# Performance work log

Hardware: AMD Instinct MI355X
Metric: run time of the kernel (lower is better)

The kernel has to match this reference:

```python
import jax, jax.numpy as jnp
import numpy as np

DEPTH = 18                     # levels 0..17 of a complete binary tree
N = 2 ** DEPTH - 1             # 262143 nodes, node n's children are 2n+1, 2n+2


def setup_inputs() -> dict:
    key = jax.random.key(0)
    ks = jax.random.split(key, 9)
    V, X, H, C = 32000, 128, 128, 5
    s = 0.05  # weight scale to keep activations in a sane range
    return {
        "x_ids": jax.random.randint(ks[0], (N,), 0, V),
        "mask": jax.random.randint(ks[1], (N,), 0, 2),
        "emb_table": jax.random.normal(ks[2], (V, X), jnp.float32),
        "W_iou": jax.random.normal(ks[3], (X, 3 * H), jnp.float32) * s,
        "U_iou": jax.random.normal(ks[4], (H, 3 * H), jnp.float32) * s,
        "b_iou": jnp.zeros((3 * H,), jnp.float32),
        "W_f": jax.random.normal(ks[5], (X, H), jnp.float32) * s,
        "U_f": jax.random.normal(ks[6], (H, H), jnp.float32) * s,
        "b_f": jnp.zeros((H,), jnp.float32),
        "W_out": jax.random.normal(ks[7], (H, C), jnp.float32) * s,
        "b_out": jnp.zeros((C,), jnp.float32),
    }


def reference(x_ids, mask, emb_table, W_iou, U_iou, b_iou, W_f, U_f, b_f, W_out, b_out):
    H = U_f.shape[0]
    # input_module: embeds = Embedding(x * mask)
    embeds = emb_table[x_ids * mask]                    # [N, X]
    # cell_module.precompute_input_values: per-node input projections
    x_iou = embeds @ W_iou + b_iou                      # [N, 3H]
    x_f = embeds @ W_f + b_f                            # [N, H]

    levels_h = [None] * DEPTH
    levels_c = [None] * DEPTH
    # dgl.prop_nodes_topo: leaves -> root, one synchronized level at a time
    for d in range(DEPTH - 1, -1, -1):
        s0, n = 2 ** d - 1, 2 ** d                      # level-d node range [s0, s0+n)
        iou = x_iou[s0:s0 + n]
        if d < DEPTH - 1:
            # children of level-d node s0+i are contiguous at level d+1: 2i, 2i+1
            h_ch = levels_h[d + 1].reshape(n, 2, H)
            c_ch = levels_c[d + 1].reshape(n, 2, H)
            iou = iou + h_ch.sum(axis=1) @ U_iou        # child-sum of h
            f = jax.nn.sigmoid(x_f[s0:s0 + n][:, None, :] + h_ch @ U_f)  # [n,2,H]
            fc = (f * c_ch).sum(axis=1)
        else:
            fc = jnp.zeros((n, H), iou.dtype)
        i, o, u = jnp.split(iou, 3, axis=-1)
        c = jax.nn.sigmoid(i) * jnp.tanh(u) + fc
        h = jax.nn.sigmoid(o) * jnp.tanh(c)
        levels_h[d] = h
        levels_c[d] = c

    h_all = jnp.concatenate(levels_h, axis=0)           # [N, H], node-index order
    # output_module: per-node linear readout
    return h_all @ W_out + b_out                        # [N, C]
```

## Files before the change

kernel.cpp:

```cpp
#include <hip/hip_runtime.h>

#define DEPTH 18
#define NN ((1 << DEPTH) - 1)

typedef __attribute__((ext_vector_type(8))) short short8;
typedef __attribute__((ext_vector_type(4))) float f32x4;

__device__ __forceinline__ float sigm_(float x) { return 1.f / (1.f + __expf(-x)); }
__device__ __forceinline__ float tanh_(float x) { float e = __expf(2.f * x); return 1.f - 2.f / (e + 1.f); }
__device__ __forceinline__ unsigned short f2bf(float f) {
    union { float f; unsigned int u; } v; v.f = f;
    unsigned int r = (v.u + 0x7fffu + ((v.u >> 16) & 1u)) >> 16;
    return (unsigned short)r;
}
__device__ __forceinline__ float bf2f(unsigned short h) {
    union { unsigned int u; float f; } v; v.u = ((unsigned int)h) << 16; return v.f;
}

__global__ void cvt_emb(const float* __restrict__ src, unsigned short* __restrict__ dst, int n4) {
    int i = blockIdx.x * 256 + threadIdx.x;
    if (i < n4) {
        float4 v = ((const float4*)src)[i];
        ushort4 o; o.x = f2bf(v.x); o.y = f2bf(v.y); o.z = f2bf(v.z); o.w = f2bf(v.w);
        ((ushort4*)dst)[i] = o;
    }
}

__global__ void build_bpack(const float* __restrict__ Wiou, const float* __restrict__ Uiou,
                            const float* __restrict__ Wf, const float* __restrict__ Uf,
                            unsigned short* __restrict__ pack) {
    int idx = blockIdx.x * 256 + threadIdx.x;
    int c = idx >> 14, r = idx & 16383, j = r >> 5, kl = r & 31;
    int k2 = c * 32 + kl;
    float v;
    if (j < 384) v = (k2 < 128) ? Wiou[k2 * 384 + j] : Uiou[(k2 - 128) * 384 + j];
    else { int jf = j - 384; v = (k2 < 128) ? Wf[k2 * 128 + jf] : Uf[(k2 - 128) * 128 + jf]; }
    pack[idx] = f2bf(v);
}

template<int HC>
__global__ __launch_bounds__(256, 2) void tree_level_mfma(
    const int* __restrict__ xids, const int* __restrict__ msk,
    const unsigned short* __restrict__ embB, const unsigned short* __restrict__ bpack,
    const float* __restrict__ biou, const float* __restrict__ bfv,
    const float* __restrict__ Wout, const float* __restrict__ bout,
    unsigned short* __restrict__ hB, float* __restrict__ c_ws, float* __restrict__ outp,
    int s0)
{
    __shared__ __align__(16) unsigned short A_s[16384];
    __shared__ __align__(16) float wout_t[660];

    const int t  = threadIdx.x;
    const int g0 = s0 + blockIdx.x * 32;

    if (t < 160) {
        float4 v = ((const float4*)Wout)[t];
        const int e0 = 4 * t;
        wout_t[((e0    ) % 5) * 132 + (e0    ) / 5] = v.x;
        wout_t[((e0 + 1) % 5) * 132 + (e0 + 1) / 5] = v.y;
        wout_t[((e0 + 2) % 5) * 132 + (e0 + 2) / 5] = v.z;
        wout_t[((e0 + 3) % 5) * 132 + (e0 + 3) / 5] = v.w;
    }

    {
        const int n = t >> 3, seg = t & 7;
        const int g = g0 + n;
        const int ei = xids[g] * msk[g];
        const uint4* es = (const uint4*)(embB + (size_t)ei * 128 + seg * 16);
        uint4 e0 = es[0], e1 = es[1];
        const int cc = seg >> 1, q0 = (seg & 1) * 2;
        *(uint4*)&A_s[(cc * 4 + q0) * 256 + n * 8]       = e0;
        *(uint4*)&A_s[(cc * 4 + q0 + 1) * 256 + n * 8]   = e1;
        if (HC) {
            const int row = t >> 2, qt = t & 3;
            const int child = 2 * g0 + 1 + row;
            const int m = row >> 1, reg = 2 + (row & 1);
            const uint4* hp = (const uint4*)(hB + (size_t)child * 128 + qt * 32);
            uint4 p0 = hp[0], p1 = hp[1], p2 = hp[2], p3 = hp[3];
            unsigned short* base = &A_s[reg * 4096 + qt * 1024 + m * 8];
            *(uint4*)(base)       = p0;
            *(uint4*)(base + 256) = p1;
            *(uint4*)(base + 512) = p2;
            *(uint4*)(base + 768) = p3;
        }
    }

    const int lane = t & 63, w = t >> 6;
    const int ln = lane & 15, q = lane >> 4;

    float clp[2][2][4], crp[2][2][4];
    if (HC) {
        #pragma unroll
        for (int rt = 0; rt < 2; ++rt)
            #pragma unroll
            for (int jt = 0; jt < 2; ++jt) {
                const int col = w * 32 + jt * 16 + ln;
                #pragma unroll
                for (int r = 0; r < 4; ++r) {
                    const int g = g0 + rt * 16 + q * 4 + r;
                    clp[rt][jt][r] = c_ws[(size_t)(2 * g + 1) * 128 + col];
                    crp[rt][jt][r] = c_ws[(size_t)(2 * g + 2) * 128 + col];
                }
            }
    }

    if (HC) {
        __syncthreads();
        const int m = t >> 3, seg = t & 7;
        const int cc = seg >> 1, q0 = (seg & 1) * 2;
        #pragma unroll
        for (int u = 0; u < 2; ++u) {
            const int idx = (cc * 4 + q0 + u) * 256 + m * 8;
            short8 l = *(short8*)&A_s[2 * 4096 + idx];
            short8 r = *(short8*)&A_s[3 * 4096 + idx];
            short8 s;
            #pragma unroll
            for (int j = 0; j < 8; ++j)
                s[j] = (short)f2bf(bf2f((unsigned short)l[j]) + bf2f((unsigned short)r[j]));
            *(short8*)&A_s[4096 + idx] = s;
        }
    }
    __syncthreads();

    const unsigned short* bp = bpack + ln * 32 + q * 8;
    const unsigned short* ap = A_s + q * 256 + ln * 8;

#define BF(c, tile) (*(const short8*)(bp + (c) * 16384 + (tile) * 512))
#define AF(r, cc, rt) (*(const short8*)(ap + (r) * 4096 + (cc) * 1024 + (rt) * 128))
#define MM(acc, a, b) acc = __builtin_amdgcn_mfma_f32_16x16x32_bf16(a, b, acc, 0, 0, 0)

    f32x4 accI[2][2] = {}, accO[2][2] = {}, accU[2][2] = {}, accFl[2][2] = {}, accFr[2][2] = {};
    const int ti = 2 * w, to = 8 + 2 * w, tu = 16 + 2 * w, tf = 24 + 2 * w;

    #pragma unroll
    for (int c = 0; c < 4; ++c) {
        short8 bI0 = BF(c, ti), bI1 = BF(c, ti + 1);
        short8 bO0 = BF(c, to), bO1 = BF(c, to + 1);
        short8 bU0 = BF(c, tu), bU1 = BF(c, tu + 1);
        short8 aE0 = AF(0, c, 0), aE1 = AF(0, c, 1);
        MM(accI[0][0], aE0, bI0); MM(accI[0][1], aE0, bI1);
        MM(accI[1][0], aE1, bI0); MM(accI[1][1], aE1, bI1);
        MM(accO[0][0], aE0, bO0); MM(accO[0][1], aE0, bO1);
        MM(accO[1][0], aE1, bO0); MM(accO[1][1], aE1, bO1);
        MM(accU[0][0], aE0, bU0); MM(accU[0][1], aE0, bU1);
        MM(accU[1][0], aE1, bU0); MM(accU[1][1], aE1, bU1);
        if (HC) {
            short8 bF0 = BF(c, tf), bF1 = BF(c, tf + 1);
            MM(accFl[0][0], aE0, bF0); MM(accFl[0][1], aE0, bF1);
            MM(accFl[1][0], aE1, bF0); MM(accFl[1][1], aE1, bF1);
        }
    }
    if (HC) {
        #pragma unroll
        for (int rt = 0; rt < 2; ++rt)
            #pragma unroll
            for (int jt = 0; jt < 2; ++jt)
                accFr[rt][jt] = accFl[rt][jt];
        #pragma unroll
        for (int c = 0; c < 4; ++c) {
            short8 bI0 = BF(4 + c, ti), bI1 = BF(4 + c, ti + 1);
            short8 bO0 = BF(4 + c, to), bO1 = BF(4 + c, to + 1);
            short8 bU0 = BF(4 + c, tu), bU1 = BF(4 + c, tu + 1);
            short8 bF0 = BF(4 + c, tf), bF1 = BF(4 + c, tf + 1);
            short8 aH0 = AF(1, c, 0), aH1 = AF(1, c, 1);
            short8 aL0 = AF(2, c, 0), aL1 = AF(2, c, 1);
            short8 aR0 = AF(3, c, 0), aR1 = AF(3, c, 1);
            MM(accI[0][0], aH0, bI0); MM(accI[0][1], aH0, bI1);
            MM(accI[1][0], aH1, bI0); MM(accI[1][1], aH1, bI1);
            MM(accO[0][0], aH0, bO0); MM(accO[0][1], aH0, bO1);
            MM(accO[1][0], aH1, bO0); MM(accO[1][1], aH1, bO1);
            MM(accU[0][0], aH0, bU0); MM(accU[0][1], aH0, bU1);
            MM(accU[1][0], aH1, bU0); MM(accU[1][1], aH1, bU1);
            MM(accFl[0][0], aL0, bF0); MM(accFl[0][1], aL0, bF1);
            MM(accFl[1][0], aL1, bF0); MM(accFl[1][1], aL1, bF1);
            MM(accFr[0][0], aR0, bF0); MM(accFr[0][1], aR0, bF1);
            MM(accFr[1][0], aR1, bF0); MM(accFr[1][1], aR1, bF1);
        }
    }
#undef BF
#undef AF

    __syncthreads();
    float* h_s = (float*)A_s;

    #pragma unroll
    for (int rt = 0; rt < 2; ++rt) {
        #pragma unroll
        for (int jt = 0; jt < 2; ++jt) {
            const int col = w * 32 + jt * 16 + ln;
            const float bib = biou[col], bob = biou[128 + col], bub = biou[256 + col];
            const float bfb = bfv[col];
            #pragma unroll
            for (int r = 0; r < 4; ++r) {
                const int row = rt * 16 + q * 4 + r;
                const int g = g0 + row;
                const float iv = accI[rt][jt][r] + bib;
                const float ov = accO[rt][jt][r] + bob;
                const float uv = accU[rt][jt][r] + bub;
                float fc = 0.f;
                if (HC) {
                    const float fl = sigm_(accFl[rt][jt][r] + bfb);
                    const float fr = sigm_(accFr[rt][jt][r] + bfb);
                    fc = fl * clp[rt][jt][r] + fr * crp[rt][jt][r];
                }
                const float cc = sigm_(iv) * tanh_(uv) + fc;
                const float hh = sigm_(ov) * tanh_(cc);
                c_ws[(size_t)g * 128 + col] = cc;
                hB[(size_t)g * 128 + col] = f2bf(hh);
                h_s[row * 132 + col] = hh;
            }
        }
    }
    __syncthreads();
    if (t < 160) {
        const int n = t / 5, cc5 = t - 5 * n;
        float acc = bout[cc5];
        const float* hp = &h_s[n * 132];
        const float* wp = &wout_t[cc5 * 132];
        #pragma unroll 4
        for (int k4 = 0; k4 < 32; ++k4) {
            float4 hv = *(const float4*)(hp + 4 * k4);
            float4 wv = *(const float4*)(wp + 4 * k4);
            acc += hv.x * wv.x + hv.y * wv.y + hv.z * wv.z + hv.w * wv.w;
        }
        outp[(size_t)(g0 + n) * 5 + cc5] = acc;
    }
}

#define MM(acc, a, b) acc = __builtin_amdgcn_mfma_f32_16x16x32_bf16(a, b, acc, 0, 0, 0)
__global__ __launch_bounds__(256) void tree_subtree(
    const int* __restrict__ xids, const int* __restrict__ msk,
    const unsigned short* __restrict__ embB, const unsigned short* __restrict__ bpack,
    const float* __restrict__ biou, const float* __restrict__ bfv,
    const float* __restrict__ Wout, const float* __restrict__ bout,
    unsigned short* __restrict__ hB, float* __restrict__ c_ws, float* __restrict__ outp,
    int dTop, int dBot)
{
    __shared__ __align__(16) unsigned short A_s[6144];
    __shared__ __align__(16) float cbuf[2][16][128];
    __shared__ __align__(16) float wout_t[5][132];

    const int t = threadIdx.x, b = blockIdx.x;
    const int lane = t & 63, w = t >> 6;
    const int ln = lane & 15, q = lane >> 4;

    if (t < 160) {
        float4 v = ((const float4*)Wout)[t];
        const int e0 = 4 * t;
        wout_t[(e0    ) % 5][(e0    ) / 5] = v.x;
        wout_t[(e0 + 1) % 5][(e0 + 1) / 5] = v.y;
        wout_t[(e0 + 2) % 5][(e0 + 2) / 5] = v.z;
        wout_t[(e0 + 3) % 5][(e0 + 3) / 5] = v.w;
    }

    const int col0 = w * 32 + ln, col1 = col0 + 16;
    const float bib0 = biou[col0], bob0 = biou[128 + col0], bub0 = biou[256 + col0], bfb0 = bfv[col0];
    const float bib1 = biou[col1], bob1 = biou[128 + col1], bub1 = biou[256 + col1], bfb1 = bfv[col1];

    const unsigned short* bp = bpack + ln * 32 + q * 8;
    const unsigned short* ap = A_s + (q * 16 + ln) * 8;
    const int ti = 2 * w, to = 8 + 2 * w, tu = 16 + 2 * w, tf = 24 + 2 * w;

    for (int d = dTop; d >= dBot; --d) {
        const int nd = 1 << (d - dBot);
        const int g0 = ((1 << d) - 1) + (b << (d - dBot));
        const int par = (dTop - d) & 1;

        if (t < 128) {
            const int m = t >> 3, seg = t & 7;
            const int g = g0 + m;
            const int ei = xids[g] * msk[g];
            const uint4* es = (const uint4*)(embB + (size_t)ei * 128 + seg * 16);
            uint4 e0 = es[0], e1 = es[1];
            const int cc = seg >> 1, q0 = (seg & 1) * 2;
            *(uint4*)&A_s[cc * 512 + (q0 * 16 + m) * 8]       = e0;
            *(uint4*)&A_s[cc * 512 + ((q0 + 1) * 16 + m) * 8] = e1;
        }
        if (d == dTop) {
            const int row = t >> 3, sg = t & 7;
            const int child = 2 * g0 + 1 + row;
            const uint4* hp = (const uint4*)(hB + (size_t)child * 128 + sg * 16);
            uint4 h0 = hp[0], h1 = hp[1];
            const int reg = 1 + (row & 1), mm = row >> 1;
            const int cc = sg >> 1, q0 = (sg & 1) * 2;
            *(uint4*)&A_s[reg * 2048 + cc * 512 + (q0 * 16 + mm) * 8]       = h0;
            *(uint4*)&A_s[reg * 2048 + cc * 512 + ((q0 + 1) * 16 + mm) * 8] = h1;
        }
        __syncthreads();

        f32x4 accI[2] = {}, accO[2] = {}, accU[2] = {}, accFl[2] = {}, accFr[2] = {};
#define BF1(c, tile) (*(const short8*)(bp + (c) * 16384 + (tile) * 512))
#define AF1(r, c) (*(const short8*)(ap + (r) * 2048 + (c) * 512))
        #pragma unroll
        for (int c = 0; c < 4; ++c) {
            short8 aE = AF1(0, c);
            MM(accI[0], aE, BF1(c, ti)); MM(accI[1], aE, BF1(c, ti + 1));
            MM(accO[0], aE, BF1(c, to)); MM(accO[1], aE, BF1(c, to + 1));
            MM(accU[0], aE, BF1(c, tu)); MM(accU[1], aE, BF1(c, tu + 1));
            MM(accFl[0], aE, BF1(c, tf)); MM(accFl[1], aE, BF1(c, tf + 1));
        }
        accFr[0] = accFl[0]; accFr[1] = accFl[1];
        #pragma unroll
        for (int c = 0; c < 4; ++c) {
            short8 aL = AF1(1, c), aR = AF1(2, c);
            short8 bI0 = BF1(4 + c, ti), bI1 = BF1(4 + c, ti + 1);
            short8 bO0 = BF1(4 + c, to), bO1 = BF1(4 + c, to + 1);
            short8 bU0 = BF1(4 + c, tu), bU1 = BF1(4 + c, tu + 1);
            short8 bF0 = BF1(4 + c, tf), bF1 = BF1(4 + c, tf + 1);
            MM(accI[0], aL, bI0); MM(accI[0], aR, bI0);
            MM(accI[1], aL, bI1); MM(accI[1], aR, bI1);
            MM(accO[0], aL, bO0); MM(accO[0], aR, bO0);
            MM(accO[1], aL, bO1); MM(accO[1], aR, bO1);
            MM(accU[0], aL, bU0); MM(accU[0], aR, bU0);
            MM(accU[1], aL, bU1); MM(accU[1], aR, bU1);
            MM(accFl[0], aL, bF0); MM(accFl[1], aL, bF1);
            MM(accFr[0], aR, bF0); MM(accFr[1], aR, bF1);
        }
#undef BF1
#undef AF1
        __syncthreads();

        #pragma unroll
        for (int jt = 0; jt < 2; ++jt) {
            const int col = jt ? col1 : col0;
            const float bib = jt ? bib1 : bib0, bob = jt ? bob1 : bob0;
            const float bub = jt ? bub1 : bub0, bfb = jt ? bfb1 : bfb0;
            const f32x4 aI = accI[jt], aO = accO[jt], aU = accU[jt];
            const f32x4 aFl = accFl[jt], aFr = accFr[jt];
            #pragma unroll
            for (int r = 0; r < 4; ++r) {
                const int row = q * 4 + r;
                const int g = g0 + row;
                float cl, cr;
                if (d == dTop) {
                    cl = c_ws[(size_t)(2 * g + 1) * 128 + col];
                    cr = c_ws[(size_t)(2 * g + 2) * 128 + col];
                } else {
                    cl = cbuf[1 - par][2 * row][col];
                    cr = cbuf[1 - par][2 * row + 1][col];
                }
                const float iv = aI[r] + bib;
                const float ov = aO[r] + bob;
                const float uv = aU[r] + bub;
                const float fl = sigm_(aFl[r] + bfb);
                const float fr = sigm_(aFr[r] + bfb);
                const float cc = sigm_(iv) * tanh_(uv) + fl * cl + fr * cr;
                const float hh = sigm_(ov) * tanh_(cc);
                cbuf[par][row][col] = cc;
                const unsigned short hb = f2bf(hh);
                const int reg = 1 + (row & 1), mm = row >> 1;
                A_s[reg * 2048 + (col >> 5) * 512 + ((((col >> 3) & 3) * 16) + mm) * 8 + (col & 7)] = hb;
                if (row < nd) {
                    c_ws[(size_t)g * 128 + col] = cc;
                    hB[(size_t)g * 128 + col] = hb;
                }
            }
        }
        __syncthreads();
        if (t < nd * 5) {
            const int n = t / 5, cc5 = t - 5 * n;
            const int reg = 1 + (n & 1), mm = n >> 1;
            float acc = bout[cc5];
            const unsigned short* hbase = &A_s[reg * 2048 + mm * 8];
            const float* wp = wout_t[cc5];
            #pragma unroll
            for (int oct = 0; oct < 16; ++oct) {
                short8 hv = *(const short8*)(hbase + (oct >> 2) * 512 + (oct & 3) * 128);
                const float* wo = wp + oct * 8;
                float4 w0 = *(const float4*)(wo);
                float4 w1 = *(const float4*)(wo + 4);
                acc += bf2f((unsigned short)hv[0]) * w0.x + bf2f((unsigned short)hv[1]) * w0.y
                     + bf2f((unsigned short)hv[2]) * w0.z + bf2f((unsigned short)hv[3]) * w0.w
                     + bf2f((unsigned short)hv[4]) * w1.x + bf2f((unsigned short)hv[5]) * w1.y
                     + bf2f((unsigned short)hv[6]) * w1.z + bf2f((unsigned short)hv[7]) * w1.w;
            }
            outp[(size_t)(g0 + n) * 5 + cc5] = acc;
        }
        __syncthreads();
    }
}
#undef MM

extern "C" void kernel_launch(void* const* d_in, const int* in_sizes, int n_in,
                              void* d_out, int out_size, void* d_ws, size_t ws_size,
                              hipStream_t stream)
{
    (void)in_sizes; (void)n_in; (void)out_size; (void)ws_size;
    const int*   xids = (const int*)d_in[0];
    const int*   msk  = (const int*)d_in[1];
    const float* emb  = (const float*)d_in[2];
    const float* Wiou = (const float*)d_in[3];
    const float* Uiou = (const float*)d_in[4];
    const float* biou = (const float*)d_in[5];
    const float* Wf   = (const float*)d_in[6];
    const float* Uf   = (const float*)d_in[7];
    const float* bfv  = (const float*)d_in[8];
    const float* Wout = (const float*)d_in[9];
    const float* bout = (const float*)d_in[10];
    float* outp = (float*)d_out;

    unsigned short* embB  = (unsigned short*)d_ws;
    unsigned short* bpack = embB + (size_t)32000 * 128;
    unsigned short* hB    = bpack + 131072;
    float*          c_ws  = (float*)(hB + (size_t)NN * 128);

    cvt_emb<<<dim3((32000 * 128 / 4 + 255) / 256), dim3(256), 0, stream>>>(emb, embB, 32000 * 128 / 4);
    build_bpack<<<dim3(131072 / 256), dim3(256), 0, stream>>>(Wiou, Uiou, Wf, Uf, bpack);

    {
        const int d = DEPTH - 1, s0 = (1 << d) - 1;
        tree_level_mfma<0><<<dim3((1 << d) / 32), dim3(256), 0, stream>>>(
            xids, msk, embB, bpack, biou, bfv, Wout, bout, hB, c_ws, outp, s0);
    }
    for (int d = DEPTH - 2; d >= 10; --d) {
        const int s0 = (1 << d) - 1;
        tree_level_mfma<1><<<dim3((1 << d) / 32), dim3(256), 0, stream>>>(
            xids, msk, embB, bpack, biou, bfv, Wout, bout, hB, c_ws, outp, s0);
    }
    tree_subtree<<<dim3(32), dim3(256), 0, stream>>>(
        xids, msk, embB, bpack, biou, bfv, Wout, bout, hB, c_ws, outp, 9, 5);
    tree_subtree<<<dim3(1), dim3(256), 0, stream>>>(
        xids, msk, embB, bpack, biou, bfv, Wout, bout, hB, c_ws, outp, 4, 0);
}
```

Measured before the change: 391.5 us.

## Fuse leaf level and level 16 into one kernel keeping leaf state in LDS

Adds a kernel that computes the 64 leaf nodes for each group of 32 level-16 parents, keeps their c in shared memory and their h as bf16 MFMA fragments in LDS, then computes the parents directly. This removes one launch and the global write/read round trip of leaf h and c. Leaf h and c are no longer written to global memory, which is safe because only the parents consume them. It also raises LDS use per block (extra 64x129 float buffer), which may lower occupancy.

```diff
diff --git a/kernel.cpp b/kernel.cpp
--- a/kernel.cpp
+++ b/kernel.cpp
@@ -36,6 +36,230 @@
     if (j < 384) v = (k2 < 128) ? Wiou[k2 * 384 + j] : Uiou[(k2 - 128) * 384 + j];
     else { int jf = j - 384; v = (k2 < 128) ? Wf[k2 * 128 + jf] : Uf[(k2 - 128) * 128 + jf]; }
     pack[idx] = f2bf(v);
+}
+
+#define MM(acc, a, b) acc = __builtin_amdgcn_mfma_f32_16x16x32_bf16(a, b, acc, 0, 0, 0)
+
+__global__ __launch_bounds__(256, 2) void tree_leaf16_fused(
+    const int* __restrict__ xids, const int* __restrict__ msk,
+    const unsigned short* __restrict__ embB, const unsigned short* __restrict__ bpack,
+    const float* __restrict__ biou, const float* __restrict__ bfv,
+    const float* __restrict__ Wout, const float* __restrict__ bout,
+    unsigned short* __restrict__ hB, float* __restrict__ c_ws, float* __restrict__ outp)
+{
+    __shared__ __align__(16) unsigned short A_s[16384];
+    __shared__ __align__(16) float c_lds[64][129];
+    __shared__ __align__(16) float wout_t[660];
+
+    const int t   = threadIdx.x;
+    const int g0p = 65535 + blockIdx.x * 32;
+    const int gl0 = 2 * g0p + 1;
+
+    if (t < 160) {
+        float4 v = ((const float4*)Wout)[t];
+        const int e0 = 4 * t;
+        wout_t[((e0    ) % 5) * 132 + (e0    ) / 5] = v.x;
+        wout_t[((e0 + 1) % 5) * 132 + (e0 + 1) / 5] = v.y;
+        wout_t[((e0 + 2) % 5) * 132 + (e0 + 2) / 5] = v.z;
+        wout_t[((e0 + 3) % 5) * 132 + (e0 + 3) / 5] = v.w;
+    }
+
+    {
+        const int n = t >> 3, seg = t & 7;
+        const int cc = seg >> 1, q0 = (seg & 1) * 2;
+        #pragma unroll
+        for (int sp = 0; sp < 2; ++sp) {
+            const int g = gl0 + sp * 32 + n;
+            const int ei = xids[g] * msk[g];
+            const uint4* es = (const uint4*)(embB + (size_t)ei * 128 + seg * 16);
+            uint4 e0 = es[0], e1 = es[1];
+            unsigned short* base = &A_s[sp * 4096];
+            *(uint4*)&base[(cc * 4 + q0) * 256 + n * 8]       = e0;
+            *(uint4*)&base[(cc * 4 + q0 + 1) * 256 + n * 8]   = e1;
+        }
+    }
+    __syncthreads();
+
+    const int lane = t & 63, w = t >> 6;
+    const int ln = lane & 15, q = lane >> 4;
+    const unsigned short* bp = bpack + ln * 32 + q * 8;
+    const unsigned short* ap = A_s + q * 256 + ln * 8;
+    const int ti = 2 * w, to = 8 + 2 * w, tu = 16 + 2 * w, tf = 24 + 2 * w;
+
+#define BF(c, tile) (*(const short8*)(bp + (c) * 16384 + (tile) * 512))
+#define AF(r, cc, rt) (*(const short8*)(ap + (r) * 4096 + (cc) * 1024 + (rt) * 128))
+
+    #pragma unroll
+    for (int sp = 0; sp < 2; ++sp) {
+        f32x4 aI[2][2] = {}, aO[2][2] = {}, aU[2][2] = {};
+        #pragma unroll
+        for (int c = 0; c < 4; ++c) {
+            short8 bI0 = BF(c, ti), bI1 = BF(c, ti + 1);
+            short8 bO0 = BF(c, to), bO1 = BF(c, to + 1);
+            short8 bU0 = BF(c, tu), bU1 = BF(c, tu + 1);
+            short8 aE0 = AF(sp, c, 0), aE1 = AF(sp, c, 1);
+            MM(aI[0][0], aE0, bI0); MM(aI[0][1], aE0, bI1);
+            MM(aI[1][0], aE1, bI0); MM(aI[1][1], aE1, bI1);
+            MM(aO[0][0], aE0, bO0); MM(aO[0][1], aE0, bO1);
+            MM(aO[1][0], aE1, bO0); MM(aO[1][1], aE1, bO1);
+            MM(aU[0][0], aE0, bU0); MM(aU[0][1], aE0, bU1);
+            MM(aU[1][0], aE1, bU0); MM(aU[1][1], aE1, bU1);
+        }
+        #pragma unroll
+        for (int rt = 0; rt < 2; ++rt) {
+            #pragma unroll
+            for (int jt = 0; jt < 2; ++jt) {
+                const int col = w * 32 + jt * 16 + ln;
+                const float bib = biou[col], bob = biou[128 + col], bub = biou[256 + col];
+                const int fragoff = ((col >> 5) * 4 + ((col >> 3) & 3)) * 256 + (col & 7);
+                #pragma unroll
+                for (int r = 0; r < 4; ++r) {
+                    const int lr = sp * 32 + rt * 16 + q * 4 + r;
+                    const float iv = aI[rt][jt][r] + bib;
+                    const float ov = aO[rt][jt][r] + bob;
+                    const float uv = aU[rt][jt][r] + bub;
+                    const float cv = sigm_(iv) * tanh_(uv);
+                    const float hv = sigm_(ov) * tanh_(cv);
+                    c_lds[lr][col] = cv;
+                    A_s[(2 + (lr & 1)) * 4096 + fragoff + (lr >> 1) * 8] = f2bf(hv);
+                }
+            }
+        }
+    }
+    __syncthreads();
+
+    {
+        const int m = t >> 3, seg = t & 7;
+        const int cc = seg >> 1, q0 = (seg & 1) * 2;
+        #pragma unroll
+        for (int u = 0; u < 2; ++u) {
+            const int idx = (cc * 4 + q0 + u) * 256 + m * 8;
+            short8 l = *(short8*)&A_s[2 * 4096 + idx];
+            short8 r = *(short8*)&A_s[3 * 4096 + idx];
+            short8 s;
+            #pragma unroll
+            for (int j = 0; j < 8; ++j)
+                s[j] = (short)f2bf(bf2f((unsigned short)l[j]) + bf2f((unsigned short)r[j]));
+            *(short8*)&A_s[4096 + idx] = s;
+        }
+        {
+            const int g = g0p + m;
+            const int ei = xids[g] * msk[g];
+            const uint4* es = (const uint4*)(embB + (size_t)ei * 128 + seg * 16);
+            uint4 e0 = es[0], e1 = es[1];
+            *(uint4*)&A_s[(cc * 4 + q0) * 256 + m * 8]       = e0;
+            *(uint4*)&A_s[(cc * 4 + q0 + 1) * 256 + m * 8]   = e1;
+        }
+        for (int o = t; o < 320; o += 256) {
+            const int n = o / 5, cc5 = o - 5 * n;
+            const int reg = 2 + (n & 1), mm = n >> 1;
+            float acc = bout[cc5];
+            const unsigned short* hbase = &A_s[reg * 4096 + mm * 8];
+            const float* wp = &wout_t[cc5 * 132];
+            #pragma unroll
+            for (int j = 0; j < 16; ++j) {
+                short8 hv = *(const short8*)(hbase + j * 256);
+                const float* wo = wp + j * 8;
+                float4 w0 = *(const float4*)(wo);
+                float4 w1 = *(const float4*)(wo + 4);
+                acc += bf2f((unsigned short)hv[0]) * w0.x + bf2f((unsigned short)hv[1]) * w0.y
+                     + bf2f((unsigned short)hv[2]) * w0.z + bf2f((unsigned short)hv[3]) * w0.w
+                     + bf2f((unsigned short)hv[4]) * w1.x + bf2f((unsigned short)hv[5]) * w1.y
+                     + bf2f((unsigned short)hv[6]) * w1.z + bf2f((unsigned short)hv[7]) * w1.w;
+            }
+            outp[(size_t)(gl0 + n) * 5 + cc5] = acc;
+        }
+    }
+    __syncthreads();
+
+    f32x4 accI[2][2] = {}, accO[2][2] = {}, accU[2][2] = {}, accFl[2][2] = {}, accFr[2][2] = {};
+
+    #pragma unroll
+    for (int c = 0; c < 4; ++c) {
+        short8 bI0 = BF(c, ti), bI1 = BF(c, ti + 1);
+        short8 bO0 = BF(c, to), bO1 = BF(c, to + 1);
+        short8 bU0 = BF(c, tu), bU1 = BF(c, tu + 1);
+        short8 aE0 = AF(0, c, 0), aE1 = AF(0, c, 1);
+        MM(accI[0][0], aE0, bI0); MM(accI[0][1], aE0, bI1);
+        MM(accI[1][0], aE1, bI0); MM(accI[1][1], aE1, bI1);
+        MM(accO[0][0], aE0, bO0); MM(accO[0][1], aE0, bO1);
+        MM(accO[1][0], aE1, bO0); MM(accO[1][1], aE1, bO1);
+        MM(accU[0][0], aE0, bU0); MM(accU[0][1], aE0, bU1);
+        MM(accU[1][0], aE1, bU0); MM(accU[1][1], aE1, bU1);
+        short8 bF0 = BF(c, tf), bF1 = BF(c, tf + 1);
+        MM(accFl[0][0], aE0, bF0); MM(accFl[0][1], aE0, bF1);
+        MM(accFl[1][0], aE1, bF0); MM(accFl[1][1], aE1, bF1);
+    }
+    #pragma unroll
+    for (int rt = 0; rt < 2; ++rt)
+        #pragma unroll
+        for (int jt = 0; jt < 2; ++jt)
+            accFr[rt][jt] = accFl[rt][jt];
+    #pragma unroll
+    for (int c = 0; c < 4; ++c) {
+        short8 bI0 = BF(4 + c, ti), bI1 = BF(4 + c, ti + 1);
+        short8 bO0 = BF(4 + c, to), bO1 = BF(4 + c, to + 1);
+        short8 bU0 = BF(4 + c, tu), bU1 = BF(4 + c, tu + 1);
+        short8 bF0 = BF(4 + c, tf), bF1 = BF(4 + c, tf + 1);
+        short8 aH0 = AF(1, c, 0), aH1 = AF(1, c, 1);
+        short8 aL0 = AF(2, c, 0), aL1 = AF(2, c, 1);
+        short8 aR0 = AF(3, c, 0), aR1 = AF(3, c, 1);
+        MM(accI[0][0], aH0, bI0); MM(accI[0][1], aH0, bI1);
+        MM(accI[1][0], aH1, bI0); MM(accI[1][1], aH1, bI1);
+        MM(accO[0][0], aH0, bO0); MM(accO[0][1], aH0, bO1);
+        MM(accO[1][0], aH1, bO0); MM(accO[1][1], aH1, bO1);
+        MM(accU[0][0], aH0, bU0); MM(accU[0][1], aH0, bU1);
+        MM(accU[1][0], aH1, bU0); MM(accU[1][1], aH1, bU1);
+        MM(accFl[0][0], aL0, bF0); MM(accFl[0][1], aL0, bF1);
+        MM(accFl[1][0], aL1, bF0); MM(accFl[1][1], aL1, bF1);
+        MM(accFr[0][0], aR0, bF0); MM(accFr[0][1], aR0, bF1);
+        MM(accFr[1][0], aR1, bF0); MM(accFr[1][1], aR1, bF1);
+    }
+#undef BF
+#undef AF
+
+    __syncthreads();
+    float* h_s = (float*)A_s;
+
+    #pragma unroll
+    for (int rt = 0; rt < 2; ++rt) {
+        #pragma unroll
+        for (int jt = 0; jt < 2; ++jt) {
+            const int col = w * 32 + jt * 16 + ln;
+            const float bib = biou[col], bob = biou[128 + col], bub = biou[256 + col];
+            const float bfb = bfv[col];
+            #pragma unroll
+            for (int r = 0; r < 4; ++r) {
+                const int row = rt * 16 + q * 4 + r;
+                const int g = g0p + row;
+                const float iv = accI[rt][jt][r] + bib;
+                const float ov = accO[rt][jt][r] + bob;
+                const float uv = accU[rt][jt][r] + bub;
+                const float fl = sigm_(accFl[rt][jt][r] + bfb);
+                const float fr = sigm_(accFr[rt][jt][r] + bfb);
+                const float fc = fl * c_lds[2 * row][col] + fr * c_lds[2 * row + 1][col];
+                const float cv = sigm_(iv) * tanh_(uv) + fc;
+                const float hv = sigm_(ov) * tanh_(cv);
+                c_ws[(size_t)g * 128 + col] = cv;
+                hB[(size_t)g * 128 + col] = f2bf(hv);
+                h_s[row * 132 + col] = hv;
+            }
+        }
+    }
+    __syncthreads();
+    if (t < 160) {
+        const int n = t / 5, cc5 = t - 5 * n;
+        float acc = bout[cc5];
+        const float* hp = &h_s[n * 132];
+        const float* wp = &wout_t[cc5 * 132];
+        #pragma unroll 4
+        for (int k4 = 0; k4 < 32; ++k4) {
+            float4 hv = *(const float4*)(hp + 4 * k4);
+            float4 wv = *(const float4*)(wp + 4 * k4);
+            acc += hv.x * wv.x + hv.y * wv.y + hv.z * wv.z + hv.w * wv.w;
+        }
+        outp[(size_t)(g0p + n) * 5 + cc5] = acc;
+    }
 }
 
 template<int HC>
@@ -127,7 +351,6 @@
 
 #define BF(c, tile) (*(const short8*)(bp + (c) * 16384 + (tile) * 512))
 #define AF(r, cc, rt) (*(const short8*)(ap + (r) * 4096 + (cc) * 1024 + (rt) * 128))
-#define MM(acc, a, b) acc = __builtin_amdgcn_mfma_f32_16x16x32_bf16(a, b, acc, 0, 0, 0)
 
     f32x4 accI[2][2] = {}, accO[2][2] = {}, accU[2][2] = {}, accFl[2][2] = {}, accFr[2][2] = {};
     const int ti = 2 * w, to = 8 + 2 * w, tu = 16 + 2 * w, tf = 24 + 2 * w;
@@ -227,7 +450,6 @@
     }
 }
 
-#define MM(acc, a, b) acc = __builtin_amdgcn_mfma_f32_16x16x32_bf16(a, b, acc, 0, 0, 0)
 __global__ __launch_bounds__(256) void tree_subtree(
     const int* __restrict__ xids, const int* __restrict__ msk,
     const unsigned short* __restrict__ embB, const unsigned short* __restrict__ bpack,
@@ -407,12 +629,10 @@
     cvt_emb<<<dim3((32000 * 128 / 4 + 255) / 256), dim3(256), 0, stream>>>(emb, embB, 32000 * 128 / 4);
     build_bpack<<<dim3(131072 / 256), dim3(256), 0, stream>>>(Wiou, Uiou, Wf, Uf, bpack);
 
-    {
-        const int d = DEPTH - 1, s0 = (1 << d) - 1;
-        tree_level_mfma<0><<<dim3((1 << d) / 32), dim3(256), 0, stream>>>(
-            xids, msk, embB, bpack, biou, bfv, Wout, bout, hB, c_ws, outp, s0);
-    }
-    for (int d = DEPTH - 2; d >= 10; --d) {
+    tree_leaf16_fused<<<dim3(2048), dim3(256), 0, stream>>>(
+        xids, msk, embB, bpack, biou, bfv, Wout, bout, hB, c_ws, outp);
+
+    for (int d = DEPTH - 3; d >= 10; --d) {
         const int s0 = (1 << d) - 1;
         tree_level_mfma<1><<<dim3((1 << d) / 32), dim3(256), 0, stream>>>(
             xids, msk, embB, bpack, biou, bfv, Wout, bout, hB, c_ws, outp, s0);
```

After: 387.0 us. About the same (-1.1%).
